# Optimization experiments

Measured on AMD Instinct MI355X. Metric: run time of the kernel, lower is better.

The kernel has to match this reference:

```python
import jax, jax.numpy as jnp
import numpy as np

N_NODES = 100000
N_EDGES = 3200000
IN_FEATS = 128
OUT_FEATS = 64


def setup_inputs() -> dict:
    key = jax.random.key(0)
    k1, k2, k3, k4 = jax.random.split(key, 4)
    features = jax.random.normal(k1, (N_NODES, IN_FEATS), dtype=jnp.float32)
    W = jax.random.normal(k2, (IN_FEATS, OUT_FEATS), dtype=jnp.float32) * (1.0 / np.sqrt(IN_FEATS))
    b = jnp.zeros((OUT_FEATS,), dtype=jnp.float32)
    src = jax.random.randint(k3, (N_EDGES,), 0, N_NODES, dtype=jnp.int32)
    dst = jax.random.randint(k4, (N_EDGES,), 0, N_NODES, dtype=jnp.int32)
    return {"features": features, "W": W, "b": b, "src": src, "dst": dst}


def reference(features, W, b, src, dst):
    # DGL GraphConv with norm='both':
    #   h = D_dst^{-1/2} * (A^T @ (D_src^{-1/2} * X @ W)) + b
    # (W applied before aggregation since in_feats > out_feats, as DGL does)
    N = features.shape[0]
    ones = jnp.ones(src.shape[0], dtype=features.dtype)
    out_deg = jax.ops.segment_sum(ones, src, num_segments=N)
    in_deg = jax.ops.segment_sum(ones, dst, num_segments=N)
    out_norm = jax.lax.rsqrt(jnp.clip(out_deg, 1.0))  # [N]
    in_norm = jax.lax.rsqrt(jnp.clip(in_deg, 1.0))    # [N]
    x = (features * out_norm[:, None]) @ W            # [N, out_feats]
    msgs = x[src]                                     # [E, out_feats] irregular gather
    agg = jax.ops.segment_sum(msgs, dst, num_segments=N)  # [N, out_feats] scatter-add
    h = agg * in_norm[:, None] + b                    # [N, out_feats]
    return h.mean(axis=1)                             # [N], mean over feature dim
```

## Files before the change

### kernel.cpp

```cpp
#include <hip/hip_runtime.h>

#define NN 100000
#define NE 3200000
#define IN_F 128
#define OUT_F 64

#define BW_SHIFT 9
#define BWIDTH 512
#define NB 196
#define CAP 20480
#define CB 500
#define EPB 6400
#define NQ (EPB / 4)

__global__ __launch_bounds__(1024) void bin_kernel(const int* __restrict__ src,
                                                   const int* __restrict__ dst,
                                                   int* __restrict__ curS_g,
                                                   int* __restrict__ curD_g,
                                                   unsigned short* __restrict__ srcloc,
                                                   int* __restrict__ pack,
                                                   const float* __restrict__ W,
                                                   const float* __restrict__ bias,
                                                   float* __restrict__ wbar,
                                                   float* __restrict__ bbar) {
    __shared__ int hs[NB], hd[NB];
    __shared__ int lS[NB], lD[NB];
    __shared__ int cS[NB], cD[NB];
    __shared__ int gS[NB], gD[NB];
    __shared__ int scanbuf[256];
    __shared__ unsigned short stS[EPB];
    __shared__ int stD[EPB];
    const int blk = blockIdx.x;
    const int t = threadIdx.x;
    for (int k = t; k < NB; k += 1024) { hs[k] = 0; hd[k] = 0; }
    __syncthreads();

    const int4* s4 = (const int4*)(src + blk * EPB);
    const int4* d4 = (const int4*)(dst + blk * EPB);
    int4 sc[2], dc[2];
    #pragma unroll
    for (int u = 0; u < 2; ++u) {
        int i = t + u * 1024;
        if (i < NQ) { sc[u] = s4[i]; dc[u] = d4[i]; }
        else        { sc[u] = make_int4(-1, -1, -1, -1); dc[u] = sc[u]; }
    }
    #pragma unroll
    for (int u = 0; u < 2; ++u) {
        if (sc[u].x >= 0) {
            atomicAdd(&hs[sc[u].x >> BW_SHIFT], 1);
            atomicAdd(&hs[sc[u].y >> BW_SHIFT], 1);
            atomicAdd(&hs[sc[u].z >> BW_SHIFT], 1);
            atomicAdd(&hs[sc[u].w >> BW_SHIFT], 1);
            atomicAdd(&hd[dc[u].x >> BW_SHIFT], 1);
            atomicAdd(&hd[dc[u].y >> BW_SHIFT], 1);
            atomicAdd(&hd[dc[u].z >> BW_SHIFT], 1);
            atomicAdd(&hd[dc[u].w >> BW_SHIFT], 1);
        }
    }
    __syncthreads();
    if (t < 256) scanbuf[t] = (t < NB) ? hs[t] : 0;
    __syncthreads();
    #pragma unroll
    for (int off = 1; off < 256; off <<= 1) {
        int x = (t < 256 && t >= off) ? scanbuf[t - off] : 0;
        __syncthreads();
        if (t < 256) scanbuf[t] += x;
        __syncthreads();
    }
    if (t < NB) { int e = scanbuf[t] - hs[t]; lS[t] = e; cS[t] = e; }
    __syncthreads();
    if (t < 256) scanbuf[t] = (t < NB) ? hd[t] : 0;
    __syncthreads();
    #pragma unroll
    for (int off = 1; off < 256; off <<= 1) {
        int x = (t < 256 && t >= off) ? scanbuf[t - off] : 0;
        __syncthreads();
        if (t < 256) scanbuf[t] += x;
        __syncthreads();
    }
    if (t < NB) { int e = scanbuf[t] - hd[t]; lD[t] = e; cD[t] = e; }
    if (t < NB) {
        gS[t] = t * CAP + atomicAdd(&curS_g[t], hs[t]);
        gD[t] = t * CAP + atomicAdd(&curD_g[t], hd[t]);
    }
    __syncthreads();
    #pragma unroll
    for (int u = 0; u < 2; ++u) {
        if (sc[u].x >= 0) {
            int p;
            p = atomicAdd(&cS[sc[u].x >> BW_SHIFT], 1); stS[p] = (unsigned short)(sc[u].x & (BWIDTH - 1));
            p = atomicAdd(&cS[sc[u].y >> BW_SHIFT], 1); stS[p] = (unsigned short)(sc[u].y & (BWIDTH - 1));
            p = atomicAdd(&cS[sc[u].z >> BW_SHIFT], 1); stS[p] = (unsigned short)(sc[u].z & (BWIDTH - 1));
            p = atomicAdd(&cS[sc[u].w >> BW_SHIFT], 1); stS[p] = (unsigned short)(sc[u].w & (BWIDTH - 1));
            p = atomicAdd(&cD[dc[u].x >> BW_SHIFT], 1); stD[p] = sc[u].x | ((dc[u].x & (BWIDTH - 1)) << 17);
            p = atomicAdd(&cD[dc[u].y >> BW_SHIFT], 1); stD[p] = sc[u].y | ((dc[u].y & (BWIDTH - 1)) << 17);
            p = atomicAdd(&cD[dc[u].z >> BW_SHIFT], 1); stD[p] = sc[u].z | ((dc[u].z & (BWIDTH - 1)) << 17);
            p = atomicAdd(&cD[dc[u].w >> BW_SHIFT], 1); stD[p] = sc[u].w | ((dc[u].w & (BWIDTH - 1)) << 17);
        }
    }
    __syncthreads();
    const int grp = t >> 4, gl = t & 15;
    for (int k = grp; k < NB; k += 64) {
        int len = hs[k], lb = lS[k], gb = gS[k];
        for (int j = gl; j < len; j += 16) srcloc[gb + j] = stS[lb + j];
        len = hd[k]; lb = lD[k]; gb = gD[k];
        for (int j = gl; j < len; j += 16) pack[gb + j] = stD[lb + j];
    }
    if (blk == 0) {
        if (t < IN_F) {
            float s = 0.f;
            for (int j = 0; j < OUT_F; ++j) s += W[t * OUT_F + j];
            wbar[t] = s * (1.0f / OUT_F);
        } else if (t == IN_F) {
            float sb = 0.f;
            for (int j = 0; j < OUT_F; ++j) sb += bias[j];
            *bbar = sb * (1.0f / OUT_F);
        }
    }
}

__global__ __launch_bounds__(1024) void bucket_scalar_kernel(const unsigned short* __restrict__ srcloc,
                                                             const int* __restrict__ curS_g,
                                                             const float* __restrict__ features,
                                                             const float* __restrict__ wbar,
                                                             float* __restrict__ sval) {
    __shared__ int cnt[BWIDTH];
    __shared__ float4 wsh[IN_F / 4];
    const int k = blockIdx.x;
    const int t = threadIdx.x;
    if (t < IN_F / 4) wsh[t] = ((const float4*)wbar)[t];
    for (int i = t; i < BWIDTH; i += 1024) cnt[i] = 0;
    __syncthreads();
    const int base = k * CAP;
    const int len = curS_g[k];
    for (int i = t; i < len; i += 1024) atomicAdd(&cnt[srcloc[base + i]], 1);
    __syncthreads();
    const int wv = t >> 6, ln = t & 63;
    const int sub = ln >> 4, sl = ln & 15;
    const float4 wa = wsh[sl], wb = wsh[sl + 16];
    #pragma unroll
    for (int it = 0; it < 8; ++it) {
        const int loc = (wv << 5) + (it << 2) + sub;
        const int node = (k << BW_SHIFT) + loc;
        if (node < NN) {
            const float4* f4 = (const float4*)(features + (size_t)node * IN_F);
            float4 fa = f4[sl], fb = f4[sl + 16];
            float p = fa.x * wa.x + fa.y * wa.y + fa.z * wa.z + fa.w * wa.w
                    + fb.x * wb.x + fb.y * wb.y + fb.z * wb.z + fb.w * wb.w;
            #pragma unroll
            for (int off = 1; off < 16; off <<= 1) p += __shfl_xor(p, off);
            if (sl == 0) sval[node] = p * rsqrtf(fmaxf((float)cnt[loc], 1.0f));
        }
    }
}

__global__ __launch_bounds__(1024) void accum_kernel(const int* __restrict__ pack,
                                                     const int* __restrict__ curD_g,
                                                     const float* __restrict__ sval,
                                                     const float* __restrict__ bbar,
                                                     float* __restrict__ out) {
    __shared__ float agg[BWIDTH];
    __shared__ int cnt[BWIDTH];
    const int k = blockIdx.x;
    const int t = threadIdx.x;
    for (int i = t; i < BWIDTH; i += 1024) { agg[i] = 0.f; cnt[i] = 0; }
    __syncthreads();
    const int base = k * CAP;
    const int len = curD_g[k];
    for (int i = t; i < len; i += 1024) {
        int p = pack[base + i];
        int s = p & 0x1FFFF;
        int loc = (p >> 17) & (BWIDTH - 1);
        float v = sval[s];
        atomicAdd(&agg[loc], v);
        atomicAdd(&cnt[loc], 1);
    }
    __syncthreads();
    for (int i = t; i < BWIDTH; i += 1024) {
        int node = (k << BW_SHIFT) + i;
        if (node < NN) out[node] = agg[i] * rsqrtf(fmaxf((float)cnt[i], 1.0f)) + bbar[0];
    }
}

__global__ void wbar_fb_kernel(const float* __restrict__ W, const float* __restrict__ bias,
                               float* __restrict__ wbar, float* __restrict__ bbar) {
    int k = threadIdx.x;
    float s = 0.f;
    for (int j = 0; j < OUT_F; ++j) s += W[k * OUT_F + j];
    wbar[k] = s * (1.0f / OUT_F);
    if (k == 0) {
        float sb = 0.f;
        for (int j = 0; j < OUT_F; ++j) sb += bias[j];
        *bbar = sb * (1.0f / OUT_F);
    }
}
__global__ void deg_kernel(const int* __restrict__ src, const int* __restrict__ dst,
                           int* __restrict__ deg_out, int* __restrict__ deg_in) {
    const int nq = NE / 4;
    int i = blockIdx.x * blockDim.x + threadIdx.x;
    const int stride = gridDim.x * blockDim.x;
    const int4* src4 = (const int4*)src;
    const int4* dst4 = (const int4*)dst;
    for (; i < nq; i += stride) {
        int4 s = src4[i];
        int4 d = dst4[i];
        atomicAdd(&deg_out[s.x], 1); atomicAdd(&deg_out[s.y], 1);
        atomicAdd(&deg_out[s.z], 1); atomicAdd(&deg_out[s.w], 1);
        atomicAdd(&deg_in[d.x], 1);  atomicAdd(&deg_in[d.y], 1);
        atomicAdd(&deg_in[d.z], 1);  atomicAdd(&deg_in[d.w], 1);
    }
}
__global__ void node_scalar_deg_kernel(const float* __restrict__ features,
                                       const int* __restrict__ deg_out,
                                       const float* __restrict__ wbar,
                                       float* __restrict__ sval) {
    const int lane = threadIdx.x & 63;
    const int wave = threadIdx.x >> 6;
    const int node = blockIdx.x * 4 + wave;
    if (node >= NN) return;
    const float2* f2 = (const float2*)(features + (size_t)node * IN_F);
    const float2* w2 = (const float2*)wbar;
    float2 f = f2[lane];
    float2 w = w2[lane];
    float p = f.x * w.x + f.y * w.y;
    #pragma unroll
    for (int off = 32; off > 0; off >>= 1) p += __shfl_down(p, off);
    if (lane == 0) {
        float d = (float)deg_out[node];
        sval[node] = p * rsqrtf(fmaxf(d, 1.0f));
    }
}
__global__ void scatter_kernel(const int* __restrict__ src, const int* __restrict__ dst,
                               const float* __restrict__ sval, float* __restrict__ agg) {
    const int nq = NE / 4;
    int i = blockIdx.x * blockDim.x + threadIdx.x;
    const int stride = gridDim.x * blockDim.x;
    const int4* src4 = (const int4*)src;
    const int4* dst4 = (const int4*)dst;
    for (; i < nq; i += stride) {
        int4 s = src4[i];
        int4 d = dst4[i];
        atomicAdd(&agg[d.x], sval[s.x]);
        atomicAdd(&agg[d.y], sval[s.y]);
        atomicAdd(&agg[d.z], sval[s.z]);
        atomicAdd(&agg[d.w], sval[s.w]);
    }
}
__global__ void final_kernel(const float* __restrict__ agg, const int* __restrict__ deg_in,
                             const float* __restrict__ bbar, float* __restrict__ out) {
    int n = blockIdx.x * blockDim.x + threadIdx.x;
    if (n >= NN) return;
    float d = (float)deg_in[n];
    out[n] = agg[n] * rsqrtf(fmaxf(d, 1.0f)) + *bbar;
}

extern "C" void kernel_launch(void* const* d_in, const int* in_sizes, int n_in,
                              void* d_out, int out_size, void* d_ws, size_t ws_size,
                              hipStream_t stream) {
    const float* features = (const float*)d_in[0];
    const float* W        = (const float*)d_in[1];
    const float* bias     = (const float*)d_in[2];
    const int*   src      = (const int*)d_in[3];
    const int*   dst      = (const int*)d_in[4];
    float* out = (float*)d_out;

    size_t need_words = (size_t)NB * CAP + (size_t)NB * CAP / 2 + 2 * NB
                      + (size_t)NN + IN_F + 1;
    if (ws_size >= need_words * 4 + 64) {
        int* w_ = (int*)d_ws;
        int*  pack              = w_;
        unsigned short* srcloc  = (unsigned short*)(w_ + (size_t)NB * CAP);
        int*  curS_g            = w_ + (size_t)NB * CAP + (size_t)NB * CAP / 2;
        int*  curD_g            = curS_g + NB;
        float* sval             = (float*)(curD_g + NB);
        float* wbar             = sval + NN;
        float* bbar             = wbar + IN_F;

        hipMemsetAsync(curS_g, 0, 2 * NB * sizeof(int), stream);
        bin_kernel<<<CB, 1024, 0, stream>>>(src, dst, curS_g, curD_g, srcloc, pack,
                                            W, bias, wbar, bbar);
        bucket_scalar_kernel<<<NB, 1024, 0, stream>>>(srcloc, curS_g, features, wbar, sval);
        accum_kernel<<<NB, 1024, 0, stream>>>(pack, curD_g, sval, bbar, out);
    } else {
        int*   deg_out = (int*)d_ws;
        int*   deg_in  = deg_out + NN;
        float* agg     = (float*)(deg_in + NN);
        float* sval    = agg + NN;
        float* wbar    = sval + NN;
        float* bbar    = wbar + IN_F;
        hipMemsetAsync(d_ws, 0, (size_t)3 * NN * sizeof(int), stream);
        wbar_fb_kernel<<<1, 128, 0, stream>>>(W, bias, wbar, bbar);
        deg_kernel<<<2048, 256, 0, stream>>>(src, dst, deg_out, deg_in);
        node_scalar_deg_kernel<<<(NN + 3) / 4, 256, 0, stream>>>(features, deg_out, wbar, sval);
        scatter_kernel<<<2048, 256, 0, stream>>>(src, dst, sval, agg);
        final_kernel<<<(NN + 255) / 256, 256, 0, stream>>>(agg, deg_in, bbar, out);
    }
}
```

Baseline: 158.3 us.

## Replicate bin histograms, use wave-shuffle scans, split bucket_scalar blocks in half

The binning kernel now keeps two privatized copies of its shared histograms to reduce atomic contention, and replaces the two barrier-heavy 256-wide Hillis-Steele scans with wave-level shuffle scans run concurrently for src and dst. The bucket_scalar kernel launches twice as many blocks, each handling half of a 512-node bucket, so more CUs take part in the feature dot-product phase. In exchange, each half-block reads the whole bucket's srcloc list and filters it, doubling that read traffic.

```diff
diff --git a/kernel.cpp b/kernel.cpp
--- a/kernel.cpp
+++ b/kernel.cpp
@@ -23,16 +23,16 @@
                                                    const float* __restrict__ bias,
                                                    float* __restrict__ wbar,
                                                    float* __restrict__ bbar) {
-    __shared__ int hs[NB], hd[NB];
+    __shared__ int hs[2][NB], hd[2][NB];
     __shared__ int lS[NB], lD[NB];
     __shared__ int cS[NB], cD[NB];
     __shared__ int gS[NB], gD[NB];
-    __shared__ int scanbuf[256];
+    __shared__ int wtot[8];
     __shared__ unsigned short stS[EPB];
     __shared__ int stD[EPB];
     const int blk = blockIdx.x;
     const int t = threadIdx.x;
-    for (int k = t; k < NB; k += 1024) { hs[k] = 0; hd[k] = 0; }
+    for (int k = t; k < 2 * NB; k += 1024) { (&hs[0][0])[k] = 0; (&hd[0][0])[k] = 0; }
     __syncthreads();
 
     const int4* s4 = (const int4*)(src + blk * EPB);
@@ -44,44 +44,51 @@
         if (i < NQ) { sc[u] = s4[i]; dc[u] = d4[i]; }
         else        { sc[u] = make_int4(-1, -1, -1, -1); dc[u] = sc[u]; }
     }
+    const int r = (t >> 9) & 1;
     #pragma unroll
     for (int u = 0; u < 2; ++u) {
         if (sc[u].x >= 0) {
-            atomicAdd(&hs[sc[u].x >> BW_SHIFT], 1);
-            atomicAdd(&hs[sc[u].y >> BW_SHIFT], 1);
-            atomicAdd(&hs[sc[u].z >> BW_SHIFT], 1);
-            atomicAdd(&hs[sc[u].w >> BW_SHIFT], 1);
-            atomicAdd(&hd[dc[u].x >> BW_SHIFT], 1);
-            atomicAdd(&hd[dc[u].y >> BW_SHIFT], 1);
-            atomicAdd(&hd[dc[u].z >> BW_SHIFT], 1);
-            atomicAdd(&hd[dc[u].w >> BW_SHIFT], 1);
-        }
-    }
-    __syncthreads();
-    if (t < 256) scanbuf[t] = (t < NB) ? hs[t] : 0;
-    __syncthreads();
-    #pragma unroll
-    for (int off = 1; off < 256; off <<= 1) {
-        int x = (t < 256 && t >= off) ? scanbuf[t - off] : 0;
-        __syncthreads();
-        if (t < 256) scanbuf[t] += x;
-        __syncthreads();
-    }
-    if (t < NB) { int e = scanbuf[t] - hs[t]; lS[t] = e; cS[t] = e; }
-    __syncthreads();
-    if (t < 256) scanbuf[t] = (t < NB) ? hd[t] : 0;
-    __syncthreads();
-    #pragma unroll
-    for (int off = 1; off < 256; off <<= 1) {
-        int x = (t < 256 && t >= off) ? scanbuf[t - off] : 0;
-        __syncthreads();
-        if (t < 256) scanbuf[t] += x;
-        __syncthreads();
-    }
-    if (t < NB) { int e = scanbuf[t] - hd[t]; lD[t] = e; cD[t] = e; }
-    if (t < NB) {
-        gS[t] = t * CAP + atomicAdd(&curS_g[t], hs[t]);
-        gD[t] = t * CAP + atomicAdd(&curD_g[t], hd[t]);
+            atomicAdd(&hs[r][sc[u].x >> BW_SHIFT], 1);
+            atomicAdd(&hs[r][sc[u].y >> BW_SHIFT], 1);
+            atomicAdd(&hs[r][sc[u].z >> BW_SHIFT], 1);
+            atomicAdd(&hs[r][sc[u].w >> BW_SHIFT], 1);
+            atomicAdd(&hd[r][dc[u].x >> BW_SHIFT], 1);
+            atomicAdd(&hd[r][dc[u].y >> BW_SHIFT], 1);
+            atomicAdd(&hd[r][dc[u].z >> BW_SHIFT], 1);
+            atomicAdd(&hd[r][dc[u].w >> BW_SHIFT], 1);
+        }
+    }
+    __syncthreads();
+    const int side = (t < 256) ? 0 : ((t < 512) ? 1 : -1);
+    const int idx = t & 255;
+    const int ln6 = t & 63;
+    int orig = 0;
+    if (side == 0 && idx < NB) orig = hs[0][idx] + hs[1][idx];
+    if (side == 1 && idx < NB) orig = hd[0][idx] + hd[1][idx];
+    int val = orig;
+    if (side >= 0) {
+        #pragma unroll
+        for (int off = 1; off < 64; off <<= 1) {
+            int x = __shfl_up(val, off);
+            if (ln6 >= off) val += x;
+        }
+        if (ln6 == 63) wtot[t >> 6] = val;
+    }
+    __syncthreads();
+    if (side >= 0) {
+        int base = 0;
+        const int w0 = side * 4, myw = t >> 6;
+        for (int w = w0; w < myw; ++w) base += wtot[w];
+        const int excl = val + base - orig;
+        if (idx < NB) {
+            if (side == 0) {
+                lS[idx] = excl; cS[idx] = excl; hs[0][idx] = orig;
+                gS[idx] = idx * CAP + atomicAdd(&curS_g[idx], orig);
+            } else {
+                lD[idx] = excl; cD[idx] = excl; hd[0][idx] = orig;
+                gD[idx] = idx * CAP + atomicAdd(&curD_g[idx], orig);
+            }
+        }
     }
     __syncthreads();
     #pragma unroll
@@ -101,9 +108,9 @@
     __syncthreads();
     const int grp = t >> 4, gl = t & 15;
     for (int k = grp; k < NB; k += 64) {
-        int len = hs[k], lb = lS[k], gb = gS[k];
+        int len = hs[0][k], lb = lS[k], gb = gS[k];
         for (int j = gl; j < len; j += 16) srcloc[gb + j] = stS[lb + j];
-        len = hd[k]; lb = lD[k]; gb = gD[k];
+        len = hd[0][k]; lb = lD[k]; gb = gD[k];
         for (int j = gl; j < len; j += 16) pack[gb + j] = stD[lb + j];
     }
     if (blk == 0) {
@@ -124,24 +131,29 @@
                                                              const float* __restrict__ features,
                                                              const float* __restrict__ wbar,
                                                              float* __restrict__ sval) {
-    __shared__ int cnt[BWIDTH];
+    __shared__ int cnt[256];
     __shared__ float4 wsh[IN_F / 4];
-    const int k = blockIdx.x;
+    const int k = blockIdx.x >> 1;
+    const int half = blockIdx.x & 1;
     const int t = threadIdx.x;
     if (t < IN_F / 4) wsh[t] = ((const float4*)wbar)[t];
-    for (int i = t; i < BWIDTH; i += 1024) cnt[i] = 0;
+    if (t < 256) cnt[t] = 0;
     __syncthreads();
     const int base = k * CAP;
     const int len = curS_g[k];
-    for (int i = t; i < len; i += 1024) atomicAdd(&cnt[srcloc[base + i]], 1);
+    const int hsel = half << 8;
+    for (int i = t; i < len; i += 1024) {
+        int l = srcloc[base + i];
+        if ((l & 256) == hsel) atomicAdd(&cnt[l & 255], 1);
+    }
     __syncthreads();
     const int wv = t >> 6, ln = t & 63;
     const int sub = ln >> 4, sl = ln & 15;
     const float4 wa = wsh[sl], wb = wsh[sl + 16];
     #pragma unroll
-    for (int it = 0; it < 8; ++it) {
-        const int loc = (wv << 5) + (it << 2) + sub;
-        const int node = (k << BW_SHIFT) + loc;
+    for (int it = 0; it < 4; ++it) {
+        const int loc256 = (wv << 4) + (it << 2) + sub;
+        const int node = (k << BW_SHIFT) + (half << 8) + loc256;
         if (node < NN) {
             const float4* f4 = (const float4*)(features + (size_t)node * IN_F);
             float4 fa = f4[sl], fb = f4[sl + 16];
@@ -149,7 +161,7 @@
                     + fb.x * wb.x + fb.y * wb.y + fb.z * wb.z + fb.w * wb.w;
             #pragma unroll
             for (int off = 1; off < 16; off <<= 1) p += __shfl_xor(p, off);
-            if (sl == 0) sval[node] = p * rsqrtf(fmaxf((float)cnt[loc], 1.0f));
+            if (sl == 0) sval[node] = p * rsqrtf(fmaxf((float)cnt[loc256], 1.0f));
         }
     }
 }
@@ -279,7 +291,7 @@
         hipMemsetAsync(curS_g, 0, 2 * NB * sizeof(int), stream);
         bin_kernel<<<CB, 1024, 0, stream>>>(src, dst, curS_g, curD_g, srcloc, pack,
                                             W, bias, wbar, bbar);
-        bucket_scalar_kernel<<<NB, 1024, 0, stream>>>(srcloc, curS_g, features, wbar, sval);
+        bucket_scalar_kernel<<<2 * NB, 1024, 0, stream>>>(srcloc, curS_g, features, wbar, sval);
         accum_kernel<<<NB, 1024, 0, stream>>>(pack, curD_g, sval, bbar, out);
     } else {
         int*   deg_out = (int*)d_ws;
```

Measured after the change: 157.1 us. About the same (-0.8%).
